# Kernel tuning notes

Hardware: AMD Instinct MI355X
Metric: run time of the kernel (lower is better)

The kernel has to match this reference:

```python
import jax, jax.numpy as jnp
import numpy as np

G = 64          # graphs in batch
NODES = 512     # nodes per graph
CAND = 2048     # edge candidates per graph
D = 256         # in_dim
H = 256         # hid_size
ENS = 2         # ensemble
N = G * NODES   # 32768 total nodes
E = G * CAND    # 131072 total candidate edges


def setup_inputs() -> dict:
    key = jax.random.key(0)
    ks = jax.random.split(key, 8)
    s = lambda fan: 1.0 / np.sqrt(fan)
    node_feat = jax.random.normal(ks[0], (N, D), jnp.float32)
    edge_candidate = jax.random.randint(ks[1], (E, 2), 0, NODES, jnp.int32)
    nnodes = jnp.full((G,), NODES, jnp.int32)
    num_edge_candidate = jnp.full((G,), CAND, jnp.int32)
    W_enc = jax.random.normal(ks[2], (D, D), jnp.float32) * s(D)
    b_enc = jnp.zeros((D,), jnp.float32)
    W1 = jax.random.normal(ks[3], (2 * D, H), jnp.float32) * s(2 * D)
    b1 = jnp.zeros((H,), jnp.float32)
    W2 = jax.random.normal(ks[4], (H, H), jnp.float32) * s(H)
    b2 = jnp.zeros((H,), jnp.float32)
    W3 = jax.random.normal(ks[5], (H, ENS), jnp.float32) * s(H)
    b3 = jnp.zeros((ENS,), jnp.float32)
    return {
        'node_feat': node_feat, 'edge_candidate': edge_candidate,
        'nnodes': nnodes, 'num_edge_candidate': num_edge_candidate,
        'W_enc': W_enc, 'b_enc': b_enc,
        'W1': W1, 'b1': b1, 'W2': W2, 'b2': b2, 'W3': W3, 'b3': b3,
    }


def reference(node_feat, edge_candidate, nnodes, num_edge_candidate,
              W_enc, b_enc, W1, b1, W2, b2, W3, b3):
    # atom encoder (linear stand-in): x [N, D]
    x = node_feat @ W_enc + b_enc
    # per-graph node offsets: [0, cumsum(nnodes)[:-1]]
    edge_rel = jnp.concatenate([jnp.zeros((1,), nnodes.dtype), jnp.cumsum(nnodes)[:-1]])
    offsets = jnp.repeat(edge_rel, num_edge_candidate,
                         total_repeat_length=edge_candidate.shape[0])
    edge_candidate_idx = edge_candidate + offsets[:, None]  # [E, 2] global indices
    # gather endpoint embeddings and concat: [E, 2D]
    h = jnp.concatenate([x[edge_candidate_idx[:, 0]], x[edge_candidate_idx[:, 1]]], axis=-1)
    # MLP: Linear+ReLU, Linear+ReLU, Linear
    h = jax.nn.relu(h @ W1 + b1)
    h = jax.nn.relu(h @ W2 + b2)
    scores = h @ W3 + b3  # [E, ENS]
    return scores, edge_candidate_idx
```

## Files before the change

kernel.cpp:

```cpp
#include <hip/hip_runtime.h>
#include <hip/hip_bf16.h>

typedef short short8 __attribute__((ext_vector_type(8)));
typedef float f32x4 __attribute__((ext_vector_type(4)));

__device__ __forceinline__ ushort f2bf(float f) {
    union { float f; unsigned u; } v; v.f = f;
    unsigned r = v.u + 0x7fff + ((v.u >> 16) & 1);
    return (ushort)(r >> 16);
}

__device__ __forceinline__ void gload_lds16(const void* g, void* l) {
    __builtin_amdgcn_global_load_lds((const __attribute__((address_space(1))) void*)g,
                                     (__attribute__((address_space(3))) void*)l, 16, 0, 0);
}


__global__ void conv_bf16_k(const float* __restrict__ in, ushort* __restrict__ out, int n4) {
    int i = blockIdx.x * blockDim.x + threadIdx.x;
    int stride = gridDim.x * blockDim.x;
    for (int j = i; j < n4; j += stride) {
        float4 v = ((const float4*)in)[j];
        ushort4 o;
        o.x = f2bf(v.x); o.y = f2bf(v.y); o.z = f2bf(v.z); o.w = f2bf(v.w);
        ((ushort4*)out)[j] = o;
    }
}

__global__ void wc_k(const float* __restrict__ We, const float* __restrict__ be,
                     const float* __restrict__ W1, const float* __restrict__ b1,
                     float* __restrict__ Wc, float* __restrict__ bc) {
    int n = threadIdx.x;
    int k = blockIdx.x;
    if (k < 512) {
        const float* werow = We + (size_t)(k & 255) * 256;
        const float* w1col = W1 + ((k >> 8) ? 256 * 256 : 0);
        float acc = 0.f;
#pragma unroll 4
        for (int d = 0; d < 256; d++)
            acc += werow[d] * w1col[(size_t)d * 256 + n];
        Wc[(size_t)k * 256 + n] = acc;
    } else {
        float acc = b1[n];
#pragma unroll 4
        for (int d = 0; d < 256; d++)
            acc += be[d] * (W1[(size_t)d * 256 + n] + W1[(size_t)(d + 256) * 256 + n]);
        bc[n] = acc;
    }
}

__global__ void pack_b_k(const float* __restrict__ W, ushort* __restrict__ out, int K) {
    int id = blockIdx.x * blockDim.x + threadIdx.x;
    if (id >= 256 * K) return;
    int j = id & 7;
    int l = (id >> 3) & 63;
    int S = (id >> 9) % (K / 32);
    int F = id / (512 * (K / 32));
    int n = F * 16 + (l & 15);
    int k = S * 32 + (l >> 4) * 8 + j;
    out[id] = f2bf(W[(size_t)k * 256 + n]);
}

__global__ void index_k(const int* __restrict__ ec,
                        const int* __restrict__ nnodes, const int* __restrict__ ncand,
                        int G, int E,
                        int* __restrict__ idx, float* __restrict__ out_idx) {
    __shared__ int snoff[257];
    __shared__ int seoff[257];
    if (threadIdx.x == 0) {
        int a = 0, b = 0;
        for (int g = 0; g < G; g++) {
            snoff[g] = a; a += nnodes[g];
            b += ncand[g]; seoff[g] = b;
        }
    }
    __syncthreads();
    int e = blockIdx.x * blockDim.x + threadIdx.x;
    if (e >= E) return;
    int lo = 0, hi = G - 1;
    while (lo < hi) {
        int mid = (lo + hi) >> 1;
        if (seoff[mid] > e) hi = mid; else lo = mid + 1;
    }
    int off = snoff[lo];
    int g0 = ec[2 * e] + off, g1 = ec[2 * e + 1] + off;
    idx[2 * e] = g0; idx[2 * e + 1] = g1;
    out_idx[2 * e] = (float)g0; out_idx[2 * e + 1] = (float)g1;
}


#define LOADB(bk, Bp, KDIV32, t)                                                            \
    _Pragma("unroll") for (int nf = 0; nf < 2; nf++)                                        \
    _Pragma("unroll") for (int kk = 0; kk < 2; kk++)                                        \
        bk[nf * 2 + kk] = *(const short8*)&Bp[((size_t)((wn * 2 + nf) * (KDIV32)            \
                                               + (t) * 2 + kk) * 64 + l) * 8];

#define COMPUTE1(bi, bk)                                                                    \
    {                                                                                       \
        short8 af[8];                                                                       \
        _Pragma("unroll") for (int mf = 0; mf < 4; mf++)                                    \
        _Pragma("unroll") for (int kk = 0; kk < 2; kk++)                                    \
            af[mf * 2 + kk] = *(const short8*)&ring[(bi) * 8192 +                           \
                (wm * 64 + mf * 16 + llo) * 64 + (((kk * 4 + lhi) ^ (llo & 7)) * 8)];       \
        __builtin_amdgcn_s_setprio(1);                                                      \
        _Pragma("unroll") for (int mf = 0; mf < 4; mf++)                                    \
        _Pragma("unroll") for (int nf = 0; nf < 2; nf++)                                    \
        _Pragma("unroll") for (int kk = 0; kk < 2; kk++)                                    \
            acc[mf][nf] = __builtin_amdgcn_mfma_f32_16x16x32_bf16(                          \
                bk[nf * 2 + kk], af[mf * 2 + kk], acc[mf][nf], 0, 0, 0);                    \
        __builtin_amdgcn_s_setprio(0);                                                      \
    }

#define COMPUTE2(t2, bk)                                                                    \
    {                                                                                       \
        short8 af[8];                                                                       \
        _Pragma("unroll") for (int mf = 0; mf < 4; mf++)                                    \
        _Pragma("unroll") for (int kk = 0; kk < 2; kk++)                                    \
            af[mf * 2 + kk] = *(const short8*)&h1lds[                                       \
                (wm * 64 + mf * 16 + llo) * 256 +                                           \
                (((t2) * 8 | ((kk * 4 + lhi) ^ (llo & 7))) * 8)];                           \
        __builtin_amdgcn_s_setprio(1);                                                      \
        _Pragma("unroll") for (int mf = 0; mf < 4; mf++)                                    \
        _Pragma("unroll") for (int nf = 0; nf < 2; nf++)                                    \
        _Pragma("unroll") for (int kk = 0; kk < 2; kk++)                                    \
            acc[mf][nf] = __builtin_amdgcn_mfma_f32_16x16x32_bf16(                          \
                bk[nf * 2 + kk], af[mf * 2 + kk], acc[mf][nf], 0, 0, 0);                    \
        __builtin_amdgcn_s_setprio(0);                                                      \
    }

#define TILE_BARRIER(n)                                                                     \
    __builtin_amdgcn_sched_barrier(0);                                                      \
    asm volatile("s_waitcnt vmcnt(" #n ")" ::: "memory");                                   \
    __builtin_amdgcn_s_barrier();                                                           \
    __builtin_amdgcn_sched_barrier(0);

__global__ __launch_bounds__(1024, 4) void fused_mlp(
    const ushort* __restrict__ nf_bf, const int* __restrict__ idx,
    const ushort* __restrict__ pk1, const float* __restrict__ bc,
    const ushort* __restrict__ pk2, const float* __restrict__ b2,
    const float* __restrict__ W3, const float* __restrict__ b3,
    float* __restrict__ scores)
{
    __shared__ __align__(16) ushort smem[36864];
    ushort* ring = smem;
    ushort* h1lds = smem;
    float* sc = (float*)&smem[32768];

    const int tid = threadIdx.x;
    const int w = tid >> 6, l = tid & 63;
    const int llo = l & 15, lhi = l >> 4;
    const int wm = w >> 3, wn = w & 7;
    const int work = ((blockIdx.x & 7) << 7) + (blockIdx.x >> 3);
    const int m0 = work * 128;

    const int srow = tid >> 3;
    const int swz = 8 * ((l & 7) ^ ((l >> 3) & 7));
    const ushort* rp0 = nf_bf + (size_t)idx[2 * (m0 + srow) + 0] * 256 + swz;
    const ushort* rp1 = nf_bf + (size_t)idx[2 * (m0 + srow) + 1] * 256 + swz;

    f32x4 acc[4][2];
#pragma unroll
    for (int mf = 0; mf < 4; mf++)
#pragma unroll
        for (int nf = 0; nf < 2; nf++) acc[mf][nf] = {0.f, 0.f, 0.f, 0.f};

    short8 bkA[4], bkB[4];

    auto stageA = [&](int bi, int t) {
        const ushort* src = ((t < 4) ? rp0 : rp1) + ((t & 3) * 64);
        gload_lds16(src, &ring[bi * 8192 + w * 512]);
    };

    stageA(0, 0);
    LOADB(bkA, pk1, 16, 0)
    stageA(1, 1);
    TILE_BARRIER(5)

#pragma unroll
    for (int t = 0; t < 8; t++) {
        if (t + 1 < 8) {
            if (t & 1) { LOADB(bkA, pk1, 16, t + 1) } else { LOADB(bkB, pk1, 16, t + 1) }
        }
        if (t + 2 < 8) stageA((t + 2) % 3, t + 2);
        if (t & 1) COMPUTE1(t % 3, bkB)
        else       COMPUTE1(t % 3, bkA)
        if (t < 6)      { TILE_BARRIER(5) }
        else if (t == 6){ TILE_BARRIER(4) }
    }

    LOADB(bkA, pk2, 8, 0)
    __syncthreads();

    {
#pragma unroll
        for (int nf = 0; nf < 2; nf++) {
            int colb = wn * 32 + nf * 16 + lhi * 4;
            float4 bv = *(const float4*)&bc[colb];
            int c = colb >> 3;
            int coff = colb & 7;
#pragma unroll
            for (int mf = 0; mf < 4; mf++) {
                int row = wm * 64 + mf * 16 + llo;
                float v0 = fmaxf(acc[mf][nf][0] + bv.x, 0.f);
                float v1 = fmaxf(acc[mf][nf][1] + bv.y, 0.f);
                float v2 = fmaxf(acc[mf][nf][2] + bv.z, 0.f);
                float v3 = fmaxf(acc[mf][nf][3] + bv.w, 0.f);
                ushort4 o;
                o.x = f2bf(v0); o.y = f2bf(v1); o.z = f2bf(v2); o.w = f2bf(v3);
                int cs = (c & 24) | ((c & 7) ^ (row & 7));
                *(ushort4*)&h1lds[row * 256 + cs * 8 + coff] = o;
            }
        }
    }
    __syncthreads();

#pragma unroll
    for (int mf = 0; mf < 4; mf++)
#pragma unroll
        for (int nf = 0; nf < 2; nf++) acc[mf][nf] = {0.f, 0.f, 0.f, 0.f};

#pragma unroll
    for (int t2 = 0; t2 < 4; t2++) {
        if (t2 + 1 < 4) {
            if (t2 & 1) { LOADB(bkA, pk2, 8, t2 + 1) } else { LOADB(bkB, pk2, 8, t2 + 1) }
        }
        if (t2 & 1) COMPUTE2(t2, bkB)
        else        COMPUTE2(t2, bkA)
    }

    float p0[4], p1[4];
#pragma unroll
    for (int mf = 0; mf < 4; mf++) { p0[mf] = 0.f; p1[mf] = 0.f; }
#pragma unroll
    for (int nf = 0; nf < 2; nf++) {
        int colb = wn * 32 + nf * 16 + lhi * 4;
        float4 b2v = *(const float4*)&b2[colb];
        float2 w3a = ((const float2*)W3)[colb + 0];
        float2 w3b = ((const float2*)W3)[colb + 1];
        float2 w3c = ((const float2*)W3)[colb + 2];
        float2 w3d = ((const float2*)W3)[colb + 3];
#pragma unroll
        for (int mf = 0; mf < 4; mf++) {
            float v0 = fmaxf(acc[mf][nf][0] + b2v.x, 0.f);
            float v1 = fmaxf(acc[mf][nf][1] + b2v.y, 0.f);
            float v2 = fmaxf(acc[mf][nf][2] + b2v.z, 0.f);
            float v3 = fmaxf(acc[mf][nf][3] + b2v.w, 0.f);
            p0[mf] += v0 * w3a.x + v1 * w3b.x + v2 * w3c.x + v3 * w3d.x;
            p1[mf] += v0 * w3a.y + v1 * w3b.y + v2 * w3c.y + v3 * w3d.y;
        }
    }
#pragma unroll
    for (int mf = 0; mf < 4; mf++) {
        p0[mf] += __shfl_xor(p0[mf], 16); p0[mf] += __shfl_xor(p0[mf], 32);
        p1[mf] += __shfl_xor(p1[mf], 16); p1[mf] += __shfl_xor(p1[mf], 32);
    }
    if (l < 16) {
#pragma unroll
        for (int mf = 0; mf < 4; mf++) {
            int r = wm * 64 + mf * 16 + l;
            sc[(wn * 128 + r) * 2 + 0] = p0[mf];
            sc[(wn * 128 + r) * 2 + 1] = p1[mf];
        }
    }
    __syncthreads();
    if (tid < 256) {
        int row = tid >> 1, j = tid & 1;
        float s = b3[j];
#pragma unroll
        for (int q = 0; q < 8; q++) s += sc[(q * 128 + row) * 2 + j];
        scores[(size_t)(m0 + row) * 2 + j] = s;
    }
}


extern "C" void kernel_launch(void* const* d_in, const int* in_sizes, int n_in,
                              void* d_out, int out_size, void* d_ws, size_t ws_size,
                              hipStream_t stream) {
    const float* node_feat = (const float*)d_in[0];
    const int* edge_candidate = (const int*)d_in[1];
    const int* nnodes = (const int*)d_in[2];
    const int* ncand = (const int*)d_in[3];
    const float* W_enc = (const float*)d_in[4];
    const float* b_enc = (const float*)d_in[5];
    const float* W1 = (const float*)d_in[6];
    const float* b1 = (const float*)d_in[7];
    const float* W2 = (const float*)d_in[8];
    const float* b2 = (const float*)d_in[9];
    const float* W3 = (const float*)d_in[10];
    const float* b3 = (const float*)d_in[11];

    const int D = 256;
    const int G = in_sizes[2];
    const int TOTN = in_sizes[0] / D;
    const int E = in_sizes[1] / 2;
    const int ENS = in_sizes[11];

    char* wsb = (char*)d_ws;
    size_t off = 0;
    auto alloc = [&](size_t bytes) -> void* {
        void* p = wsb + off;
        off += (bytes + 255) & ~(size_t)255;
        return p;
    };
    ushort* nf_bf = (ushort*)alloc((size_t)TOTN * D * 2);
    float*  Wc    = (float*)alloc((size_t)512 * 256 * 4);
    float*  bc    = (float*)alloc(256 * 4);
    ushort* pk1   = (ushort*)alloc((size_t)512 * 256 * 2);
    ushort* pk2   = (ushort*)alloc((size_t)256 * 256 * 2);
    int* idxb     = (int*)alloc((size_t)E * 2 * 4);

    float* scores_out = (float*)d_out;
    float* idx_out = scores_out + (size_t)E * ENS;

    conv_bf16_k<<<2048, 256, 0, stream>>>(node_feat, nf_bf, TOTN * D / 4);
    wc_k<<<513, 256, 0, stream>>>(W_enc, b_enc, W1, b1, Wc, bc);
    pack_b_k<<<(256 * 512) / 256, 256, 0, stream>>>(Wc, pk1, 512);
    pack_b_k<<<(256 * 256) / 256, 256, 0, stream>>>(W2, pk2, 256);
    index_k<<<(E + 255) / 256, 256, 0, stream>>>(edge_candidate, nnodes, ncand, G, E, idxb, idx_out);

    fused_mlp<<<E / 128, 1024, 0, stream>>>(nf_bf, idxb, pk1, bc, pk2, b2, W3, b3, scores_out);
}
```

Before: 94.84 us.

## Merge prep kernels into one launch and deepen A-tile ring to four stages

```diff
diff --git a/kernel.cpp b/kernel.cpp
--- a/kernel.cpp
+++ b/kernel.cpp
@@ -16,76 +16,79 @@
 }
 
 
-__global__ void conv_bf16_k(const float* __restrict__ in, ushort* __restrict__ out, int n4) {
-    int i = blockIdx.x * blockDim.x + threadIdx.x;
-    int stride = gridDim.x * blockDim.x;
-    for (int j = i; j < n4; j += stride) {
-        float4 v = ((const float4*)in)[j];
-        ushort4 o;
-        o.x = f2bf(v.x); o.y = f2bf(v.y); o.z = f2bf(v.z); o.w = f2bf(v.w);
-        ((ushort4*)out)[j] = o;
-    }
-}
-
-__global__ void wc_k(const float* __restrict__ We, const float* __restrict__ be,
-                     const float* __restrict__ W1, const float* __restrict__ b1,
-                     float* __restrict__ Wc, float* __restrict__ bc) {
-    int n = threadIdx.x;
-    int k = blockIdx.x;
-    if (k < 512) {
-        const float* werow = We + (size_t)(k & 255) * 256;
-        const float* w1col = W1 + ((k >> 8) ? 256 * 256 : 0);
-        float acc = 0.f;
+__global__ __launch_bounds__(256) void prep_k(
+    const float* __restrict__ node_feat, ushort* __restrict__ nf_bf, int n4,
+    const int* __restrict__ ec, const int* __restrict__ nnodes, const int* __restrict__ ncand,
+    int G, int E, int* __restrict__ idxb, float* __restrict__ out_idx,
+    const float* __restrict__ W2, ushort* __restrict__ pk2,
+    const float* __restrict__ We, const float* __restrict__ be,
+    const float* __restrict__ W1, const float* __restrict__ b1,
+    ushort* __restrict__ pk1, float* __restrict__ bc)
+{
+    const int b = blockIdx.x;
+    if (b < 2048) {
+        int i = b * 256 + threadIdx.x;
+        const int stride = 2048 * 256;
+        for (int j = i; j < n4; j += stride) {
+            float4 v = ((const float4*)node_feat)[j];
+            ushort4 o;
+            o.x = f2bf(v.x); o.y = f2bf(v.y); o.z = f2bf(v.z); o.w = f2bf(v.w);
+            ((ushort4*)nf_bf)[j] = o;
+        }
+    } else if (b < 2560) {
+        __shared__ int snoff[257];
+        __shared__ int seoff[257];
+        if (threadIdx.x == 0) {
+            int a = 0, c = 0;
+            for (int g = 0; g < G; g++) {
+                snoff[g] = a; a += nnodes[g];
+                c += ncand[g]; seoff[g] = c;
+            }
+        }
+        __syncthreads();
+        int e = (b - 2048) * 256 + threadIdx.x;
+        if (e >= E) return;
+        int lo = 0, hi = G - 1;
+        while (lo < hi) {
+            int mid = (lo + hi) >> 1;
+            if (seoff[mid] > e) hi = mid; else lo = mid + 1;
+        }
+        int off = snoff[lo];
+        int g0 = ec[2 * e] + off, g1 = ec[2 * e + 1] + off;
+        idxb[2 * e] = g0; idxb[2 * e + 1] = g1;
+        out_idx[2 * e] = (float)g0; out_idx[2 * e + 1] = (float)g1;
+    } else if (b < 2816) {
+        int id = (b - 2560) * 256 + threadIdx.x;
+        int j = id & 7;
+        int l = (id >> 3) & 63;
+        int S = (id >> 9) & 7;
+        int F = id >> 12;
+        int n = F * 16 + (l & 15);
+        int k = S * 32 + (l >> 4) * 8 + j;
+        pk2[id] = f2bf(W2[(size_t)k * 256 + n]);
+    } else {
+        int k = b - 2816;
+        int n = threadIdx.x;
+        if (k < 512) {
+            const float* werow = We + (size_t)(k & 255) * 256;
+            const float* w1col = W1 + ((k >> 8) ? 256 * 256 : 0);
+            float acc = 0.f;
 #pragma unroll 4
-        for (int d = 0; d < 256; d++)
-            acc += werow[d] * w1col[(size_t)d * 256 + n];
-        Wc[(size_t)k * 256 + n] = acc;
-    } else {
-        float acc = b1[n];
+            for (int d = 0; d < 256; d++)
+                acc += werow[d] * w1col[(size_t)d * 256 + n];
+            int j = k & 7;
+            int S = k >> 5;
+            int F = n >> 4;
+            int l = ((k >> 3) & 3) * 16 + (n & 15);
+            pk1[((size_t)(F * 16 + S) * 64 + l) * 8 + j] = f2bf(acc);
+        } else {
+            float acc = b1[n];
 #pragma unroll 4
-        for (int d = 0; d < 256; d++)
-            acc += be[d] * (W1[(size_t)d * 256 + n] + W1[(size_t)(d + 256) * 256 + n]);
-        bc[n] = acc;
-    }
-}
-
-__global__ void pack_b_k(const float* __restrict__ W, ushort* __restrict__ out, int K) {
-    int id = blockIdx.x * blockDim.x + threadIdx.x;
-    if (id >= 256 * K) return;
-    int j = id & 7;
-    int l = (id >> 3) & 63;
-    int S = (id >> 9) % (K / 32);
-    int F = id / (512 * (K / 32));
-    int n = F * 16 + (l & 15);
-    int k = S * 32 + (l >> 4) * 8 + j;
-    out[id] = f2bf(W[(size_t)k * 256 + n]);
-}
-
-__global__ void index_k(const int* __restrict__ ec,
-                        const int* __restrict__ nnodes, const int* __restrict__ ncand,
-                        int G, int E,
-                        int* __restrict__ idx, float* __restrict__ out_idx) {
-    __shared__ int snoff[257];
-    __shared__ int seoff[257];
-    if (threadIdx.x == 0) {
-        int a = 0, b = 0;
-        for (int g = 0; g < G; g++) {
-            snoff[g] = a; a += nnodes[g];
-            b += ncand[g]; seoff[g] = b;
-        }
-    }
-    __syncthreads();
-    int e = blockIdx.x * blockDim.x + threadIdx.x;
-    if (e >= E) return;
-    int lo = 0, hi = G - 1;
-    while (lo < hi) {
-        int mid = (lo + hi) >> 1;
-        if (seoff[mid] > e) hi = mid; else lo = mid + 1;
-    }
-    int off = snoff[lo];
-    int g0 = ec[2 * e] + off, g1 = ec[2 * e + 1] + off;
-    idx[2 * e] = g0; idx[2 * e + 1] = g1;
-    out_idx[2 * e] = (float)g0; out_idx[2 * e + 1] = (float)g1;
+            for (int d = 0; d < 256; d++)
+                acc += be[d] * (W1[(size_t)d * 256 + n] + W1[(size_t)(d + 256) * 256 + n]);
+            bc[n] = acc;
+        }
+    }
 }
 
 
@@ -155,8 +158,9 @@
 
     const int srow = tid >> 3;
     const int swz = 8 * ((l & 7) ^ ((l >> 3) & 7));
-    const ushort* rp0 = nf_bf + (size_t)idx[2 * (m0 + srow) + 0] * 256 + swz;
-    const ushort* rp1 = nf_bf + (size_t)idx[2 * (m0 + srow) + 1] * 256 + swz;
+    const int2 ip = *(const int2*)&idx[2 * (m0 + srow)];
+    const ushort* rp0 = nf_bf + (size_t)ip.x * 256 + swz;
+    const ushort* rp1 = nf_bf + (size_t)ip.y * 256 + swz;
 
     f32x4 acc[4][2];
 #pragma unroll
@@ -174,18 +178,21 @@
     stageA(0, 0);
     LOADB(bkA, pk1, 16, 0)
     stageA(1, 1);
-    TILE_BARRIER(5)
+    stageA(2, 2);
+    TILE_BARRIER(6)
 
 #pragma unroll
     for (int t = 0; t < 8; t++) {
         if (t + 1 < 8) {
             if (t & 1) { LOADB(bkA, pk1, 16, t + 1) } else { LOADB(bkB, pk1, 16, t + 1) }
         }
-        if (t + 2 < 8) stageA((t + 2) % 3, t + 2);
-        if (t & 1) COMPUTE1(t % 3, bkB)
-        else       COMPUTE1(t % 3, bkA)
-        if (t < 6)      { TILE_BARRIER(5) }
-        else if (t == 6){ TILE_BARRIER(4) }
+        if (t + 3 < 8) stageA((t + 3) & 3, t + 3);
+        if (t & 1) COMPUTE1(t & 3, bkB)
+        else       COMPUTE1(t & 3, bkA)
+        if (t == 0)      { TILE_BARRIER(6) }
+        else if (t <= 4) { TILE_BARRIER(10) }
+        else if (t == 5) { TILE_BARRIER(9) }
+        else if (t == 6) { TILE_BARRIER(8) }
     }
 
     LOADB(bkA, pk2, 8, 0)
@@ -303,20 +310,19 @@
         return p;
     };
     ushort* nf_bf = (ushort*)alloc((size_t)TOTN * D * 2);
-    float*  Wc    = (float*)alloc((size_t)512 * 256 * 4);
-    float*  bc    = (float*)alloc(256 * 4);
     ushort* pk1   = (ushort*)alloc((size_t)512 * 256 * 2);
     ushort* pk2   = (ushort*)alloc((size_t)256 * 256 * 2);
+    float*  bc    = (float*)alloc(256 * 4);
     int* idxb     = (int*)alloc((size_t)E * 2 * 4);
 
     float* scores_out = (float*)d_out;
     float* idx_out = scores_out + (size_t)E * ENS;
 
-    conv_bf16_k<<<2048, 256, 0, stream>>>(node_feat, nf_bf, TOTN * D / 4);
-    wc_k<<<513, 256, 0, stream>>>(W_enc, b_enc, W1, b1, Wc, bc);
-    pack_b_k<<<(256 * 512) / 256, 256, 0, stream>>>(Wc, pk1, 512);
-    pack_b_k<<<(256 * 256) / 256, 256, 0, stream>>>(W2, pk2, 256);
-    index_k<<<(E + 255) / 256, 256, 0, stream>>>(edge_candidate, nnodes, ncand, G, E, idxb, idx_out);
+    prep_k<<<3329, 256, 0, stream>>>(
+        node_feat, nf_bf, TOTN * D / 4,
+        edge_candidate, nnodes, ncand, G, E, idxb, idx_out,
+        W2, pk2,
+        W_enc, b_enc, W1, b1, pk1, bc);
 
     fused_mlp<<<E / 128, 1024, 0, stream>>>(nf_bf, idxb, pk1, bc, pk2, b2, W3, b3, scores_out);
 }
```

After: 81.71 us. -13.8%, faster.
